# Performance work log

Hardware: AMD Instinct MI355X
Metric: run time of the kernel (lower is better)

The kernel has to match this reference:

```python
import jax, jax.numpy as jnp
import numpy as np

B, S, A, C, M, CE = 2, 8, 24000, 80, 20, 7
POS_TH, NEG_TH = 0.5, 0.4
V0, V1 = 0.1, 0.2              # SSD encode variances
SL1_BETA = 1.0 / 9.0
ALPHA, GAMMA = 0.25, 2.0
CB_BETA = 0.9999
EPS = 1e-7


def point_form(cf):
    # (cx,cy,w,h) -> (x1,y1,x2,y2)
    return jnp.concatenate([cf[..., :2] - cf[..., 2:] * 0.5, cf[..., :2] + cf[..., 2:] * 0.5], -1)


def jaccard(a, b):
    # a: [M,4], b: [A,4] point form -> IoU [M,A]
    lt = jnp.maximum(a[:, None, :2], b[None, :, :2])
    rb = jnp.minimum(a[:, None, 2:], b[None, :, 2:])
    wh = jnp.clip(rb - lt, 0.0)
    inter = wh[..., 0] * wh[..., 1]
    aa = (a[:, 2] - a[:, 0]) * (a[:, 3] - a[:, 1])
    ab = (b[:, 2] - b[:, 0]) * (b[:, 3] - b[:, 1])
    return inter / (aa[:, None] + ab[None, :] - inter + 1e-10)


def encode(matched, anchors_cf):
    # matched: [A,4] point form gt, anchors_cf: [A,4] center form
    g_cxcy = ((matched[:, :2] + matched[:, 2:]) * 0.5 - anchors_cf[:, :2]) / (V0 * anchors_cf[:, 2:])
    g_wh = jnp.log(jnp.clip(matched[:, 2:] - matched[:, :2], 1e-6) / anchors_cf[:, 2:]) / V1
    return jnp.concatenate([g_cxcy, g_wh], -1)


def bce(p, y):
    p = jnp.clip(p, EPS, 1.0 - EPS)
    return -(y * jnp.log(p) + (1.0 - y) * jnp.log1p(-p))


def match_one(gtb, gtl, count, anchors_pf, anchors_cf):
    # SSD-style match with ignore band: conf in {-1 ignore, 0 background, i+1 positive matched to gt i}
    valid = jnp.arange(M) < count
    iou = jnp.where(valid[:, None], jaccard(gtb, anchors_pf), -1.0)  # [M,A]
    best_prior_idx = jnp.argmax(iou, axis=1)                         # best anchor per gt
    best_truth_iou = jnp.max(iou, axis=0)                            # best gt per anchor
    best_truth_idx = jnp.argmax(iou, axis=0)
    sidx = jnp.where(valid, best_prior_idx, A)                       # out-of-range -> dropped
    best_truth_iou = best_truth_iou.at[sidx].set(2.0, mode='drop')   # force each gt's best anchor positive
    best_truth_idx = best_truth_idx.at[sidx].set(jnp.arange(M), mode='drop')
    conf = (best_truth_idx + 1).astype(jnp.int32)                    # dummy labels = gt index
    conf = jnp.where(best_truth_iou < POS_TH, -1, conf)
    conf = jnp.where(best_truth_iou < NEG_TH, 0, conf)
    loc = encode(gtb[best_truth_idx], anchors_cf)
    has = count > 0
    conf = jnp.where(has, conf, -1)                                  # empty frame -> all ignore
    loc = jnp.where(has, loc, 0.0)
    # gather per-anchor multi-hot labels: labels_bs = [zeros; gt_labels][dumy_conf]
    lab = jnp.where((conf > 0)[:, None], gtl[jnp.clip(conf - 1, 0, M - 1)], 0.0)
    return conf, loc, lab


def setup_inputs() -> dict:
    key = jax.random.key(0)
    ks = jax.random.split(key, 10)
    confidence = jax.random.normal(ks[0], (B, S, A, C), jnp.float32)
    predicted_locations = jax.random.normal(ks[1], (B, S, A, 4), jnp.float32)
    gc = jax.random.uniform(ks[2], (B, S, M, 2))
    gw = jax.random.uniform(ks[3], (B, S, M, 2), minval=0.05, maxval=0.4)
    gt_boxes = jnp.clip(jnp.concatenate([gc - gw * 0.5, gc + gw * 0.5], -1), 0.0, 1.0)
    gt_labels = (jax.random.uniform(ks[4], (B, S, M, C)) < 0.05).astype(jnp.float32)
    counts = jax.random.randint(ks[5], (B, S), 0, M + 1, jnp.int32)
    ac = jax.random.uniform(ks[6], (A, 2))
    aw = jax.random.uniform(ks[7], (A, 2), minval=0.02, maxval=0.3)
    anchors = jnp.concatenate([ac, aw], -1)  # center form (cx,cy,w,h)
    ego_preds = jax.random.normal(ks[8], (B, S, CE), jnp.float32)
    ego_labels = jax.random.randint(ks[9], (B, S), 0, CE, jnp.int32)
    cls_num_list = jax.random.randint(jax.random.fold_in(key, 11), (C,), 1, 10000, jnp.int32)
    return {"confidence": confidence, "predicted_locations": predicted_locations,
            "gt_boxes": gt_boxes, "gt_labels": gt_labels, "counts": counts,
            "anchors": anchors, "ego_preds": ego_preds, "ego_labels": ego_labels,
            "cls_num_list": cls_num_list}


def reference(confidence, predicted_locations, gt_boxes, gt_labels, counts, anchors, ego_preds, ego_labels, cls_num_list):
    preds = jax.nn.sigmoid(confidence)
    anchors_pf = point_form(anchors)
    flat = lambda x: x.reshape((B * S,) + x.shape[2:])
    conf_t, loc_t, lab_t = jax.vmap(match_one, in_axes=(0, 0, 0, None, None))(
        flat(gt_boxes), flat(gt_labels), counts.reshape(-1), anchors_pf, anchors)
    labels_bin = jax.lax.stop_gradient(conf_t.reshape(B, S, A).astype(jnp.float32))
    gt_locations = jax.lax.stop_gradient(loc_t.reshape(B, S, A, 4))
    all_labels = jax.lax.stop_gradient(lab_t.reshape(B, S, A, C))

    pos = (labels_bin > 0).astype(jnp.float32)
    num_pos = jnp.maximum(1.0, pos.sum())
    n = jnp.abs(predicted_locations - gt_locations)
    sl1 = jnp.where(n < SL1_BETA, 0.5 * n * n / SL1_BETA, n - 0.5 * SL1_BETA)
    regression_loss = (sl1 * pos[..., None]).sum() / (num_pos * 4.0)

    # class-balanced focal loss (module hardcodes gamma=1 inside sigmoid_cb_focal_loss)
    cmask = (labels_bin > -1).astype(jnp.float32)[..., None]
    w = (1.0 - CB_BETA) / (1.0 - jnp.power(jnp.float32(CB_BETA), cls_num_list.astype(jnp.float32)))
    w = w / w.sum()
    y = all_labels
    pt = preds * y + (1.0 - preds) * (1.0 - y)
    cb = w * y + (1.0 - CB_BETA) * (1.0 - y)
    cls_loss = (bce(preds, y) * cb * (1.0 - pt) * cmask).sum() / num_pos

    # ego focal loss (replicates original get_one_hot_labels column semantics)
    ep = jax.nn.sigmoid(ego_preds)
    evalid = ego_labels > -1
    col = (jnp.where(evalid[..., None], jax.nn.one_hot(ego_labels, CE), 0.0).sum((0, 1)) > 0).astype(jnp.float32)
    oh = jnp.broadcast_to(col, ep.shape)
    af = ALPHA * oh + (1.0 - ALPHA) * (1.0 - oh)
    ept = ep * oh + (1.0 - ep) * (1.0 - oh)
    n_ego = evalid.sum().astype(jnp.float32)
    ego_sum = (bce(ep, oh) * af * (1.0 - ept) ** GAMMA * evalid[..., None].astype(jnp.float32)).sum()
    ego_loss = jnp.where(n_ego > 0, ego_sum / jnp.maximum(n_ego, 1.0), 0.0)

    return regression_loss, cls_loss / 8.0 + ego_loss / 4.0
```

## Files before the change

### kernel.cpp

```cpp
#include <hip/hip_runtime.h>
#include <math.h>

#define NB 2
#define NS 8
#define NA 24000
#define NC 80
#define NM 20
#define NCE 7
#define NBS (NB*NS)
#define CPB 64
#define APC (NA/CPB)

#define POS_TH 0.5f
#define NEG_TH 0.4f
#define OMB 1e-4f

__device__ inline unsigned long long packKey(float f, unsigned idx) {
    unsigned u = __float_as_uint(f);
    u = (u & 0x80000000u) ? ~u : (u | 0x80000000u);
    return ((unsigned long long)u << 32) | (unsigned long long)(0xFFFFFFFFu - idx);
}

__global__ void __launch_bounds__(256)
k_iou(const float* __restrict__ gtb, const int* __restrict__ counts,
      const float* __restrict__ anchors,
      float* __restrict__ bt_iou, int* __restrict__ bt_idx,
      unsigned long long* __restrict__ chunkbest,
      double* __restrict__ acc, int* __restrict__ npos) {
    int bid = blockIdx.x;
    int bs = bid / CPB;
    int chunk = bid % CPB;
    int t = threadIdx.x;
    int cnt = counts[bs];

    if (bid == 0 && t == 0) { acc[0] = 0.0; acc[1] = 0.0; *npos = 0; }

    __shared__ float sg[NM][5];
    if (t < NM) {
        const float* g = gtb + ((size_t)bs * NM + t) * 4;
        float x1 = g[0], y1 = g[1], x2 = g[2], y2 = g[3];
        sg[t][0] = x1; sg[t][1] = y1; sg[t][2] = x2; sg[t][3] = y2;
        sg[t][4] = (x2 - x1) * (y2 - y1);
    }
    __syncthreads();

    unsigned long long bp[NM];
    #pragma unroll
    for (int m = 0; m < NM; m++) bp[m] = 0ULL;

    int a0 = chunk * APC;
    for (int a = a0 + t; a < a0 + APC; a += 256) {
        float4 cf = ((const float4*)anchors)[a];
        float ax1 = cf.x - cf.z * 0.5f, ay1 = cf.y - cf.w * 0.5f;
        float ax2 = cf.x + cf.z * 0.5f, ay2 = cf.y + cf.w * 0.5f;
        float aarea = (ax2 - ax1) * (ay2 - ay1);
        float best = -1.0f; int bm = 0;
        #pragma unroll
        for (int m = 0; m < NM; m++) {
            if (m < cnt) {
                float ltx = fmaxf(sg[m][0], ax1), lty = fmaxf(sg[m][1], ay1);
                float rbx = fminf(sg[m][2], ax2), rby = fminf(sg[m][3], ay2);
                float wx = fmaxf(rbx - ltx, 0.0f), wy = fmaxf(rby - lty, 0.0f);
                float inter = wx * wy;
                float iou = inter / (sg[m][4] + aarea - inter + 1e-10f);
                if (iou > best) { best = iou; bm = m; }
                unsigned long long k = packKey(iou, (unsigned)a);
                if (k > bp[m]) bp[m] = k;
            }
        }
        bt_iou[(size_t)bs * NA + a] = best;
        bt_idx[(size_t)bs * NA + a] = bm;
    }

    __shared__ unsigned long long sk[4][NM];
    int wave = t >> 6, lane = t & 63;
    for (int m = 0; m < cnt; m++) {
        unsigned long long k = bp[m];
        #pragma unroll
        for (int off = 32; off > 0; off >>= 1) {
            unsigned long long o = __shfl_xor(k, off);
            if (o > k) k = o;
        }
        if (lane == 0) sk[wave][m] = k;
    }
    __syncthreads();
    if (t < NM) {
        unsigned long long k = 0ULL;
        if (t < cnt) {
            k = sk[0][t];
            if (sk[1][t] > k) k = sk[1][t];
            if (sk[2][t] > k) k = sk[2][t];
            if (sk[3][t] > k) k = sk[3][t];
        }
        chunkbest[bid * NM + t] = k;
    }
}

__global__ void __launch_bounds__(256)
k_match(const float* __restrict__ gtb, const int* __restrict__ counts,
        const float* __restrict__ anchors, const float* __restrict__ ploc,
        const float* __restrict__ gtl, const float* __restrict__ logits,
        const int* __restrict__ cls_num,
        const unsigned long long* __restrict__ chunkbest,
        const float* __restrict__ bt_iou, const int* __restrict__ bt_idx,
        double* __restrict__ acc, int* __restrict__ npos) {
    int bid = blockIdx.x;
    int bs = bid / CPB;
    int chunk = bid % CPB;
    int t = threadIdx.x;
    int cnt = counts[bs];

    __shared__ float sg[NM][4];
    __shared__ unsigned abest[NM];
    __shared__ float wsh[NC];
    __shared__ float wsum_sh;
    if (t < NM) {
        const float* g = gtb + ((size_t)bs * NM + t) * 4;
        sg[t][0] = g[0]; sg[t][1] = g[1]; sg[t][2] = g[2]; sg[t][3] = g[3];
    }
    if (t < NC) {
        float n = (float)cls_num[t];
        wsh[t] = OMB / (1.0f - powf(0.9999f, n));
    }
    if (t < NM && t < cnt) {
        unsigned long long k = 0ULL;
        for (int c = 0; c < CPB; c++) {
            unsigned long long o = chunkbest[(bs * CPB + c) * NM + t];
            if (o > k) k = o;
        }
        abest[t] = 0xFFFFFFFFu - (unsigned)(k & 0xFFFFFFFFull);
    }
    __syncthreads();
    if (t == 0) {
        float s = 0.0f;
        for (int c = 0; c < NC; c++) s += wsh[c];
        wsum_sh = s;
    }
    __syncthreads();
    if (t < NC) wsh[t] = wsh[t] / wsum_sh;
    __syncthreads();

    const float SL1B = 1.0f / 9.0f;
    float regsum = 0.0f, possum = 0.0f, bgsum = 0.0f;
    int pcnt = 0;
    int a0 = chunk * APC;
    for (int a = a0 + t; a < a0 + APC; a += 256) {
        size_t ia = (size_t)bs * NA + a;
        float iou = bt_iou[ia];
        int idx = bt_idx[ia];
        for (int m = 0; m < cnt; m++) {
            if (abest[m] == (unsigned)a) { iou = 2.0f; idx = m; }
        }
        int code;
        if (cnt == 0) code = -1;
        else if (iou < NEG_TH) code = 0;
        else if (iou < POS_TH) code = -1;
        else code = idx + 1;

        if (code == 0) {
            const float4* xrow = (const float4*)(logits + ia * NC);
            #pragma unroll 5
            for (int c4 = 0; c4 < NC / 4; c4++) {
                float4 x4 = xrow[c4];
                float xv[4] = {x4.x, x4.y, x4.z, x4.w};
                #pragma unroll
                for (int j = 0; j < 4; j++) {
                    float x = xv[j];
                    float e = __expf(-x);
                    float s = 1.0f + e;
                    float pr = __builtin_amdgcn_rcpf(s);
                    float ls = __logf(s);
                    bgsum += (x + ls) * pr;
                }
            }
        } else if (code > 0) {
            pcnt++;
            float4 cf = ((const float4*)anchors)[a];
            float mx1 = sg[idx][0], my1 = sg[idx][1], mx2 = sg[idx][2], my2 = sg[idx][3];
            float g0 = ((mx1 + mx2) * 0.5f - cf.x) / (0.1f * cf.z);
            float g1 = ((my1 + my2) * 0.5f - cf.y) / (0.1f * cf.w);
            float g2 = logf(fmaxf(mx2 - mx1, 1e-6f) / cf.z) / 0.2f;
            float g3 = logf(fmaxf(my2 - my1, 1e-6f) / cf.w) / 0.2f;
            float4 p = ((const float4*)ploc)[ia];
            float n0 = fabsf(p.x - g0), n1 = fabsf(p.y - g1);
            float n2 = fabsf(p.z - g2), n3 = fabsf(p.w - g3);
            float s0 = n0 < SL1B ? 0.5f * n0 * n0 / SL1B : n0 - 0.5f * SL1B;
            float s1 = n1 < SL1B ? 0.5f * n1 * n1 / SL1B : n1 - 0.5f * SL1B;
            float s2 = n2 < SL1B ? 0.5f * n2 * n2 / SL1B : n2 - 0.5f * SL1B;
            float s3 = n3 < SL1B ? 0.5f * n3 * n3 / SL1B : n3 - 0.5f * SL1B;
            regsum += s0 + s1 + s2 + s3;

            const float4* yrow = (const float4*)(gtl + ((size_t)(bs * NM + idx)) * NC);
            const float4* xrow = (const float4*)(logits + ia * NC);
            #pragma unroll 5
            for (int c4 = 0; c4 < NC / 4; c4++) {
                float4 y4 = yrow[c4];
                float4 x4 = xrow[c4];
                float yv[4] = {y4.x, y4.y, y4.z, y4.w};
                float xv[4] = {x4.x, x4.y, x4.z, x4.w};
                #pragma unroll
                for (int j = 0; j < 4; j++) {
                    float x = xv[j];
                    float e = __expf(-x);
                    float s = 1.0f + e;
                    float pr = __builtin_amdgcn_rcpf(s);
                    float ls = __logf(s);
                    if (yv[j] > 0.5f) possum += ls * wsh[c4 * 4 + j] * (e * pr);
                    else              bgsum += (x + ls) * pr;
                }
            }
        }
    }
    float clssum = possum + OMB * bgsum;

    #pragma unroll
    for (int off = 32; off > 0; off >>= 1) {
        regsum += __shfl_xor(regsum, off);
        clssum += __shfl_xor(clssum, off);
        pcnt   += __shfl_xor(pcnt, off);
    }
    __shared__ float sf[4], sc[4];
    __shared__ int   si[4];
    int wave = t >> 6, lane = t & 63;
    if (lane == 0) { sf[wave] = regsum; sc[wave] = clssum; si[wave] = pcnt; }
    __syncthreads();
    if (t == 0) {
        atomicAdd(&acc[0], (double)(sf[0] + sf[1] + sf[2] + sf[3]));
        atomicAdd(&acc[1], (double)(sc[0] + sc[1] + sc[2] + sc[3]));
        atomicAdd(npos, si[0] + si[1] + si[2] + si[3]);
    }
}

__global__ void k_final(const float* __restrict__ ego_preds, const int* __restrict__ ego_labels,
                        const double* __restrict__ acc, const int* __restrict__ npos,
                        float* __restrict__ out) {
    __shared__ float scol[NCE];
    __shared__ float sred[128];
    __shared__ int   sval[128];
    const float EPSF = 1e-7f;
    int t = threadIdx.x;
    if (t < NCE) {
        float c = 0.0f;
        for (int i = 0; i < NBS; i++) {
            int l = ego_labels[i];
            if (l > -1 && l == t) c = 1.0f;
        }
        scol[t] = c;
    }
    __syncthreads();

    float term = 0.0f;
    if (t < NBS * NCE) {
        int bs = t / NCE, e = t % NCE;
        int lbl = ego_labels[bs];
        if (lbl > -1) {
            float x = ego_preds[t];
            float ep = 1.0f / (1.0f + expf(-x));
            float oh = scol[e];
            float af = 0.25f * oh + 0.75f * (1.0f - oh);
            float ept = ep * oh + (1.0f - ep) * (1.0f - oh);
            float epc = fminf(fmaxf(ep, EPSF), 1.0f - EPSF);
            float bce = -(oh * logf(epc) + (1.0f - oh) * log1pf(-epc));
            float om = 1.0f - ept;
            term = bce * af * om * om;
        }
    }
    sred[t] = term;
    sval[t] = (t < NBS && ego_labels[t] > -1) ? 1 : 0;
    __syncthreads();
    for (int off = 64; off > 0; off >>= 1) {
        if (t < off) { sred[t] += sred[t + off]; sval[t] += sval[t + off]; }
        __syncthreads();
    }
    if (t == 0) {
        float esum = sred[0];
        int ne = sval[0];
        float ego = (ne > 0) ? esum / (float)(ne > 1 ? ne : 1) : 0.0f;
        double npd = (double)(*npos);
        if (npd < 1.0) npd = 1.0;
        out[0] = (float)(acc[0] / (npd * 4.0));
        out[1] = (float)(acc[1] / npd / 8.0 + (double)ego / 4.0);
    }
}

extern "C" void kernel_launch(void* const* d_in, const int* in_sizes, int n_in,
                              void* d_out, int out_size, void* d_ws, size_t ws_size,
                              hipStream_t stream) {
    const float* confidence = (const float*)d_in[0];
    const float* ploc       = (const float*)d_in[1];
    const float* gtb        = (const float*)d_in[2];
    const float* gtl        = (const float*)d_in[3];
    const int*   counts     = (const int*)d_in[4];
    const float* anchors    = (const float*)d_in[5];
    const float* ego_preds  = (const float*)d_in[6];
    const int*   ego_labels = (const int*)d_in[7];
    const int*   cls_num    = (const int*)d_in[8];
    float* out = (float*)d_out;

    char* ws = (char*)d_ws;
    double* acc  = (double*)ws;
    int* npos    = (int*)(ws + 16);
    unsigned long long* chunkbest = (unsigned long long*)(ws + 64);
    float* bt_iou = (float*)(ws + 64 + 163840);
    int*   bt_idx = (int*)(ws + 64 + 163840 + 1536000);

    k_iou<<<NBS * CPB, 256, 0, stream>>>(gtb, counts, anchors, bt_iou, bt_idx,
                                         chunkbest, acc, npos);
    k_match<<<NBS * CPB, 256, 0, stream>>>(gtb, counts, anchors, ploc, gtl, confidence,
                                           cls_num, chunkbest, bt_iou, bt_idx, acc, npos);
    k_final<<<1, 128, 0, stream>>>(ego_preds, ego_labels, acc, npos, out);
}
```

Baseline: 284.1 us.

## Coalesce logits reads by splitting match and classification loss into two passes

Anchor codes and matched indices are first stored in shared memory. A second loop then strides over the chunk's logits as contiguous float4 elements, so adjacent threads read adjacent memory instead of each thread walking its own 320-byte row. This targets uncoalesced global loads in the dominant logits traffic. It adds shared memory, a block barrier and a per-element integer divide.

```diff
diff --git a/kernel.cpp b/kernel.cpp
--- a/kernel.cpp
+++ b/kernel.cpp
@@ -10,6 +10,7 @@
 #define NBS (NB*NS)
 #define CPB 64
 #define APC (NA/CPB)
+#define F4PC (APC*NC/4)
 
 #define POS_TH 0.5f
 #define NEG_TH 0.4f
@@ -114,6 +115,8 @@
     __shared__ unsigned abest[NM];
     __shared__ float wsh[NC];
     __shared__ float wsum_sh;
+    __shared__ int scode[APC];
+    __shared__ int sidx[APC];
     if (t < NM) {
         const float* g = gtb + ((size_t)bs * NM + t) * 4;
         sg[t][0] = g[0]; sg[t][1] = g[1]; sg[t][2] = g[2]; sg[t][3] = g[3];
@@ -138,13 +141,13 @@
     }
     __syncthreads();
     if (t < NC) wsh[t] = wsh[t] / wsum_sh;
-    __syncthreads();
 
     const float SL1B = 1.0f / 9.0f;
-    float regsum = 0.0f, possum = 0.0f, bgsum = 0.0f;
+    float regsum = 0.0f;
     int pcnt = 0;
     int a0 = chunk * APC;
-    for (int a = a0 + t; a < a0 + APC; a += 256) {
+    for (int al = t; al < APC; al += 256) {
+        int a = a0 + al;
         size_t ia = (size_t)bs * NA + a;
         float iou = bt_iou[ia];
         int idx = bt_idx[ia];
@@ -156,24 +159,9 @@
         else if (iou < NEG_TH) code = 0;
         else if (iou < POS_TH) code = -1;
         else code = idx + 1;
-
-        if (code == 0) {
-            const float4* xrow = (const float4*)(logits + ia * NC);
-            #pragma unroll 5
-            for (int c4 = 0; c4 < NC / 4; c4++) {
-                float4 x4 = xrow[c4];
-                float xv[4] = {x4.x, x4.y, x4.z, x4.w};
-                #pragma unroll
-                for (int j = 0; j < 4; j++) {
-                    float x = xv[j];
-                    float e = __expf(-x);
-                    float s = 1.0f + e;
-                    float pr = __builtin_amdgcn_rcpf(s);
-                    float ls = __logf(s);
-                    bgsum += (x + ls) * pr;
-                }
-            }
-        } else if (code > 0) {
+        scode[al] = code;
+        sidx[al] = idx;
+        if (code > 0) {
             pcnt++;
             float4 cf = ((const float4*)anchors)[a];
             float mx1 = sg[idx][0], my1 = sg[idx][1], mx2 = sg[idx][2], my2 = sg[idx][3];
@@ -189,25 +177,44 @@
             float s2 = n2 < SL1B ? 0.5f * n2 * n2 / SL1B : n2 - 0.5f * SL1B;
             float s3 = n3 < SL1B ? 0.5f * n3 * n3 / SL1B : n3 - 0.5f * SL1B;
             regsum += s0 + s1 + s2 + s3;
-
-            const float4* yrow = (const float4*)(gtl + ((size_t)(bs * NM + idx)) * NC);
-            const float4* xrow = (const float4*)(logits + ia * NC);
-            #pragma unroll 5
-            for (int c4 = 0; c4 < NC / 4; c4++) {
-                float4 y4 = yrow[c4];
-                float4 x4 = xrow[c4];
-                float yv[4] = {y4.x, y4.y, y4.z, y4.w};
-                float xv[4] = {x4.x, x4.y, x4.z, x4.w};
-                #pragma unroll
-                for (int j = 0; j < 4; j++) {
-                    float x = xv[j];
-                    float e = __expf(-x);
-                    float s = 1.0f + e;
-                    float pr = __builtin_amdgcn_rcpf(s);
-                    float ls = __logf(s);
-                    if (yv[j] > 0.5f) possum += ls * wsh[c4 * 4 + j] * (e * pr);
-                    else              bgsum += (x + ls) * pr;
-                }
+        }
+    }
+    __syncthreads();
+
+    const float4* x4p = (const float4*)logits;
+    const float4* y4p = (const float4*)gtl;
+    size_t base4 = ((size_t)bs * NA + a0) * (NC / 4);
+    float possum = 0.0f, bgsum = 0.0f;
+    for (int i = t; i < F4PC; i += 256) {
+        int al = i / 20;
+        int code = scode[al];
+        if (code == -1) continue;
+        float4 x4 = x4p[base4 + i];
+        float xv[4] = {x4.x, x4.y, x4.z, x4.w};
+        if (code > 0) {
+            int c4 = i - al * 20;
+            int idx = sidx[al];
+            float4 y4 = y4p[(bs * NM + idx) * 20 + c4];
+            float yv[4] = {y4.x, y4.y, y4.z, y4.w};
+            #pragma unroll
+            for (int j = 0; j < 4; j++) {
+                float x = xv[j];
+                float e = __expf(-x);
+                float s = 1.0f + e;
+                float pr = __builtin_amdgcn_rcpf(s);
+                float ls = __logf(s);
+                if (yv[j] > 0.5f) possum += ls * wsh[c4 * 4 + j] * (e * pr);
+                else              bgsum += (x + ls) * pr;
+            }
+        } else {
+            #pragma unroll
+            for (int j = 0; j < 4; j++) {
+                float x = xv[j];
+                float e = __expf(-x);
+                float s = 1.0f + e;
+                float pr = __builtin_amdgcn_rcpf(s);
+                float ls = __logf(s);
+                bgsum += (x + ls) * pr;
             }
         }
     }
```

New measurement: 274.3 us. -3.4%, faster.

## Stream background logits block-wide with a shared mask, correct positives separately

Applied to the files above, without the earlier changes.

The per-anchor background loss loop, which made each thread read its own 80-float logit row, is replaced by a block-wide coalesced sweep over the chunk's logits. Each anchor's inclusion is weighted by a mask kept in shared memory. Positive anchors now add only a correction term for classes whose label is positive, and those logits are read only where a label is set. The chunk count rises from 64 to 75 so each chunk's float4 count is an exact multiple of the 256-thread sweep, and the workspace offsets are shifted to match. The change targets uncoalesced row-wise loads and divergence between background and positive threads, at the cost of computing the transcendentals for ignored anchors too.

```diff
diff --git a/kernel.cpp b/kernel.cpp
--- a/kernel.cpp
+++ b/kernel.cpp
@@ -8,8 +8,9 @@
 #define NM 20
 #define NCE 7
 #define NBS (NB*NS)
-#define CPB 64
+#define CPB 75
 #define APC (NA/CPB)
+#define F4PC (APC*NC/4)
 
 #define POS_TH 0.5f
 #define NEG_TH 0.4f
@@ -114,6 +115,7 @@
     __shared__ unsigned abest[NM];
     __shared__ float wsh[NC];
     __shared__ float wsum_sh;
+    __shared__ float smask[APC];
     if (t < NM) {
         const float* g = gtb + ((size_t)bs * NM + t) * 4;
         sg[t][0] = g[0]; sg[t][1] = g[1]; sg[t][2] = g[2]; sg[t][3] = g[3];
@@ -138,13 +140,13 @@
     }
     __syncthreads();
     if (t < NC) wsh[t] = wsh[t] / wsum_sh;
-    __syncthreads();
 
     const float SL1B = 1.0f / 9.0f;
-    float regsum = 0.0f, possum = 0.0f, bgsum = 0.0f;
+    float regsum = 0.0f, corrsum = 0.0f;
     int pcnt = 0;
     int a0 = chunk * APC;
-    for (int a = a0 + t; a < a0 + APC; a += 256) {
+    for (int al = t; al < APC; al += 256) {
+        int a = a0 + al;
         size_t ia = (size_t)bs * NA + a;
         float iou = bt_iou[ia];
         int idx = bt_idx[ia];
@@ -156,24 +158,8 @@
         else if (iou < NEG_TH) code = 0;
         else if (iou < POS_TH) code = -1;
         else code = idx + 1;
-
-        if (code == 0) {
-            const float4* xrow = (const float4*)(logits + ia * NC);
-            #pragma unroll 5
-            for (int c4 = 0; c4 < NC / 4; c4++) {
-                float4 x4 = xrow[c4];
-                float xv[4] = {x4.x, x4.y, x4.z, x4.w};
-                #pragma unroll
-                for (int j = 0; j < 4; j++) {
-                    float x = xv[j];
-                    float e = __expf(-x);
-                    float s = 1.0f + e;
-                    float pr = __builtin_amdgcn_rcpf(s);
-                    float ls = __logf(s);
-                    bgsum += (x + ls) * pr;
-                }
-            }
-        } else if (code > 0) {
+        smask[al] = (code == -1) ? 0.0f : 1.0f;
+        if (code > 0) {
             pcnt++;
             float4 cf = ((const float4*)anchors)[a];
             float mx1 = sg[idx][0], my1 = sg[idx][1], mx2 = sg[idx][2], my2 = sg[idx][3];
@@ -192,26 +178,60 @@
 
             const float4* yrow = (const float4*)(gtl + ((size_t)(bs * NM + idx)) * NC);
             const float4* xrow = (const float4*)(logits + ia * NC);
-            #pragma unroll 5
+            #pragma unroll 4
             for (int c4 = 0; c4 < NC / 4; c4++) {
                 float4 y4 = yrow[c4];
-                float4 x4 = xrow[c4];
-                float yv[4] = {y4.x, y4.y, y4.z, y4.w};
-                float xv[4] = {x4.x, x4.y, x4.z, x4.w};
-                #pragma unroll
-                for (int j = 0; j < 4; j++) {
-                    float x = xv[j];
-                    float e = __expf(-x);
-                    float s = 1.0f + e;
-                    float pr = __builtin_amdgcn_rcpf(s);
-                    float ls = __logf(s);
-                    if (yv[j] > 0.5f) possum += ls * wsh[c4 * 4 + j] * (e * pr);
-                    else              bgsum += (x + ls) * pr;
+                if (y4.x > 0.5f || y4.y > 0.5f || y4.z > 0.5f || y4.w > 0.5f) {
+                    float4 x4 = xrow[c4];
+                    float yv[4] = {y4.x, y4.y, y4.z, y4.w};
+                    float xv[4] = {x4.x, x4.y, x4.z, x4.w};
+                    #pragma unroll
+                    for (int j = 0; j < 4; j++) {
+                        if (yv[j] > 0.5f) {
+                            float x = xv[j];
+                            float e = __expf(-x);
+                            float s = 1.0f + e;
+                            float pr = __builtin_amdgcn_rcpf(s);
+                            float ls = __logf(s);
+                            corrsum += ls * wsh[c4 * 4 + j] * (e * pr)
+                                     - OMB * (x + ls) * pr;
+                        }
+                    }
                 }
             }
         }
     }
-    float clssum = possum + OMB * bgsum;
+    __syncthreads();
+
+    const float4* x4p = (const float4*)logits + ((size_t)bs * NA + a0) * (NC / 4);
+    float bgsum = 0.0f;
+    #pragma unroll
+    for (int g = 0; g < 5; g++) {
+        float4 xs[5];
+        float  ms[5];
+        #pragma unroll
+        for (int j = 0; j < 5; j++) {
+            int i = t + (g * 5 + j) * 256;
+            ms[j] = smask[i / 20];
+            xs[j] = x4p[i];
+        }
+        #pragma unroll
+        for (int j = 0; j < 5; j++) {
+            float xv[4] = {xs[j].x, xs[j].y, xs[j].z, xs[j].w};
+            float tsum = 0.0f;
+            #pragma unroll
+            for (int jj = 0; jj < 4; jj++) {
+                float x = xv[jj];
+                float e = __expf(-x);
+                float s = 1.0f + e;
+                float pr = __builtin_amdgcn_rcpf(s);
+                float ls = __logf(s);
+                tsum += (x + ls) * pr;
+            }
+            bgsum = fmaf(ms[j], tsum, bgsum);
+        }
+    }
+    float clssum = corrsum + OMB * bgsum;
 
     #pragma unroll
     for (int off = 32; off > 0; off >>= 1) {
@@ -301,8 +321,8 @@
     double* acc  = (double*)ws;
     int* npos    = (int*)(ws + 16);
     unsigned long long* chunkbest = (unsigned long long*)(ws + 64);
-    float* bt_iou = (float*)(ws + 64 + 163840);
-    int*   bt_idx = (int*)(ws + 64 + 163840 + 1536000);
+    float* bt_iou = (float*)(ws + 64 + 192000);
+    int*   bt_idx = (int*)(ws + 64 + 192000 + 1536000);
 
     k_iou<<<NBS * CPB, 256, 0, stream>>>(gtb, counts, anchors, bt_iou, bt_idx,
                                          chunkbest, acc, npos);
```

Result: faster. 270.7 us (-4.7%).
